# Optimization experiments

Measured on AMD Instinct MI355X. Metric: run time of the kernel, lower is better.

The kernel has to match this reference:

```python
import jax, jax.numpy as jnp
import numpy as np

# Rational/asymptotic approximations for J0, J1 (Abramowitz & Stegun 9.4.x,
# as used in Numerical Recipes), then upward recurrence J2 = (2/x) J1 - J0.
# This reproduces scipy.special.jv(2, x) to ~1e-7 relative accuracy in fp32.

_TWO_OVER_PI = 0.636619772  # 2/pi


def _bessj0(x):
    ax = jnp.abs(x)
    y = x * x
    num = 57568490574.0 + y * (-13362590354.0 + y * (651619640.7
          + y * (-11214424.18 + y * (77392.33017 + y * (-184.9052456)))))
    den = 57568490411.0 + y * (1029532985.0 + y * (9494680.718
          + y * (59272.64853 + y * (267.8532712 + y))))
    small = num / den  # |x| < 8

    ax_safe = jnp.maximum(ax, 1e-20)
    z = 8.0 / ax_safe
    yy = z * z
    xx = ax_safe - 0.785398164  # ax - pi/4
    p1 = 1.0 + yy * (-0.1098628627e-2 + yy * (0.2734510407e-4
         + yy * (-0.2073370639e-5 + yy * 0.2093887211e-6)))
    p2 = -0.1562499995e-1 + yy * (0.1430488765e-3 + yy * (-0.6911147651e-5
         + yy * (0.7621095161e-6 + yy * (-0.934935152e-7))))
    big = jnp.sqrt(_TWO_OVER_PI / ax_safe) * (jnp.cos(xx) * p1 - z * jnp.sin(xx) * p2)
    return jnp.where(ax < 8.0, small, big)


def _bessj1(x):
    ax = jnp.abs(x)
    y = x * x
    num = x * (72362614232.0 + y * (-7895059235.0 + y * (242396853.1
          + y * (-2972611.439 + y * (15704.48260 + y * (-30.16036606))))))
    den = 144725228442.0 + y * (2300535178.0 + y * (18583304.74
          + y * (99447.43394 + y * (376.9991397 + y))))
    small = num / den  # |x| < 8

    ax_safe = jnp.maximum(ax, 1e-20)
    z = 8.0 / ax_safe
    yy = z * z
    xx = ax_safe - 2.356194491  # ax - 3*pi/4
    p1 = 1.0 + yy * (0.183105e-2 + yy * (-0.3516396496e-4
         + yy * (0.2457520174e-5 + yy * (-0.240337019e-6))))
    p2 = 0.04687499995 + yy * (-0.2002690873e-3 + yy * (0.8449199096e-5
         + yy * (-0.88228987e-6 + yy * 0.105787412e-6)))
    big = jnp.sign(x) * jnp.sqrt(_TWO_OVER_PI / ax_safe) * (
        jnp.cos(xx) * p1 - z * jnp.sin(xx) * p2)
    return jnp.where(ax < 8.0, small, big)


def _bessj2(x):
    # J2(x) = (2/x) J1(x) - J0(x); near 0 use leading series J2 ~ x^2/8.
    eps = 1e-4
    ax = jnp.abs(x)
    x_safe = jnp.where(ax < eps, 1.0, x)
    rec = (2.0 / x_safe) * _bessj1(x_safe) - _bessj0(x_safe)
    series = x * x / 8.0
    return jnp.where(ax < eps, series, rec)


def setup_inputs() -> dict:
    key = jax.random.key(0)
    # ~67M elements, 268 MB fp32 -> memory-bound elementwise map
    x = jax.random.uniform(key, (64, 1048576), dtype=jnp.float32,
                           minval=0.0, maxval=30.0)
    return {"x": x}


def reference(x):
    # Original module with type='j2': elementwise jv(2, x)
    return _bessj2(x)
```

## Files before the change

### kernel.cpp

```cpp
#include <hip/hip_runtime.h>


__device__ __forceinline__ float bessj2_fast(float x) {
    float u = 0.25f * x * x;
    float s;
    s = 2.39471e-20f;
    s = fmaf(s, u, -4.02324e-18f);
    s = fmaf(s, u,  5.75284e-16f);
    s = fmaf(s, u, -6.90369e-14f);
    s = fmaf(s, u,  6.83465e-12f);
    s = fmaf(s, u, -5.46772e-10f);
    s = fmaf(s, u,  3.44466e-08f);
    s = fmaf(s, u, -1.65344e-06f);
    s = fmaf(s, u,  5.78704e-05f);
    s = fmaf(s, u, -1.38889e-03f);
    s = fmaf(s, u,  2.08333e-02f);
    s = fmaf(s, u, -1.66667e-01f);
    s = fmaf(s, u,  0.5f);
    float j2_small = u * s;

    float xb   = fmaxf(x, 8.0f);
    float rinv = __builtin_amdgcn_rcpf(xb);
    float z    = 8.0f * rinv;
    float yy   = z * z;
    float amp  = __builtin_amdgcn_sqrtf(0.636619772f * rinv);
    float chi  = xb - 3.92699082f;
    float sc, cc;
    __sincosf(chi, &sc, &cc);
    float p = fmaf(yy, fmaf(yy,  7.74472e-05f, -1.28173828e-02f), 1.0f);
    float q = z * fmaf(yy, fmaf(yy, -1.57318e-05f, 6.00815e-04f), 0.234375f);
    float j2_big = amp * fmaf(cc, p, -(sc * q));

    return (x < 8.0f) ? j2_small : j2_big;
}

__global__ __launch_bounds__(256)
void j2_vec4_kernel(const float* __restrict__ in, float* __restrict__ out,
                    int n4) {
    const float4* in4  = reinterpret_cast<const float4*>(in);
    float4*       out4 = reinterpret_cast<float4*>(out);
    int idx    = blockIdx.x * blockDim.x + threadIdx.x;
    int stride = gridDim.x * blockDim.x;
    for (int i = idx; i < n4; i += stride) {
        float4 v = in4[i];
        float4 r;
        r.x = bessj2_fast(v.x);
        r.y = bessj2_fast(v.y);
        r.z = bessj2_fast(v.z);
        r.w = bessj2_fast(v.w);
        out4[i] = r;
    }
}

__global__ __launch_bounds__(256)
void j2_tail_kernel(const float* __restrict__ in, float* __restrict__ out,
                    int start, int n) {
    int i = start + blockIdx.x * blockDim.x + threadIdx.x;
    if (i < n) out[i] = bessj2_fast(in[i]);
}

extern "C" void kernel_launch(void* const* d_in, const int* in_sizes, int n_in,
                              void* d_out, int out_size, void* d_ws, size_t ws_size,
                              hipStream_t stream) {
    const float* in  = (const float*)d_in[0];
    float*       out = (float*)d_out;
    int n  = in_sizes[0];
    int n4 = n >> 2;

    if (n4 > 0) {
        int blocks = (n4 + 255) / 256;
        if (blocks > 2048) blocks = 2048;
        j2_vec4_kernel<<<blocks, 256, 0, stream>>>(in, out, n4);
    }
    int rem_start = n4 << 2;
    int rem = n - rem_start;
    if (rem > 0) {
        j2_tail_kernel<<<(rem + 255) / 256, 256, 0, stream>>>(in, out,
                                                              rem_start, n);
    }
}
```

Measured before the change: 105.3 us.

## Use nontemporal vector loads/stores, unroll grid-stride loop by two, fold rcp+sqrt into rsq

Switches the streaming loads and stores to nontemporal builtins on native vector types, so the data passes through without polluting caches. The grid-stride loop now processes two float4 chunks per iteration, giving more loads in flight per thread. The amplitude computation replaces a reciprocal plus square root with a single reciprocal square root, and the reciprocal is recovered by squaring it. The rsq-based reciprocal may differ slightly in rounding, and the unroll adds register pressure.

```diff
diff --git a/kernel.cpp b/kernel.cpp
--- a/kernel.cpp
+++ b/kernel.cpp
@@ -1,5 +1,7 @@
 #include <hip/hip_runtime.h>
 
+
+typedef float vf4 __attribute__((ext_vector_type(4)));
 
 __device__ __forceinline__ float bessj2_fast(float x) {
     float u = 0.25f * x * x;
@@ -20,10 +22,11 @@
     float j2_small = u * s;
 
     float xb   = fmaxf(x, 8.0f);
-    float rinv = __builtin_amdgcn_rcpf(xb);
+    float r    = __builtin_amdgcn_rsqf(xb);
+    float rinv = r * r;
+    float amp  = 0.797884561f * r;
     float z    = 8.0f * rinv;
     float yy   = z * z;
-    float amp  = __builtin_amdgcn_sqrtf(0.636619772f * rinv);
     float chi  = xb - 3.92699082f;
     float sc, cc;
     __sincosf(chi, &sc, &cc);
@@ -34,21 +37,35 @@
     return (x < 8.0f) ? j2_small : j2_big;
 }
 
+__device__ __forceinline__ vf4 j2_vec(vf4 v) {
+    vf4 r;
+    r.x = bessj2_fast(v.x);
+    r.y = bessj2_fast(v.y);
+    r.z = bessj2_fast(v.z);
+    r.w = bessj2_fast(v.w);
+    return r;
+}
+
 __global__ __launch_bounds__(256)
 void j2_vec4_kernel(const float* __restrict__ in, float* __restrict__ out,
                     int n4) {
-    const float4* in4  = reinterpret_cast<const float4*>(in);
-    float4*       out4 = reinterpret_cast<float4*>(out);
+    const vf4* in4  = reinterpret_cast<const vf4*>(in);
+    vf4*       out4 = reinterpret_cast<vf4*>(out);
     int idx    = blockIdx.x * blockDim.x + threadIdx.x;
     int stride = gridDim.x * blockDim.x;
-    for (int i = idx; i < n4; i += stride) {
-        float4 v = in4[i];
-        float4 r;
-        r.x = bessj2_fast(v.x);
-        r.y = bessj2_fast(v.y);
-        r.z = bessj2_fast(v.z);
-        r.w = bessj2_fast(v.w);
-        out4[i] = r;
+
+    int i = idx;
+    for (; i + stride < n4; i += 2 * stride) {
+        vf4 a = __builtin_nontemporal_load(in4 + i);
+        vf4 b = __builtin_nontemporal_load(in4 + i + stride);
+        vf4 ra = j2_vec(a);
+        vf4 rb = j2_vec(b);
+        __builtin_nontemporal_store(ra, out4 + i);
+        __builtin_nontemporal_store(rb, out4 + i + stride);
+    }
+    if (i < n4) {
+        vf4 a = __builtin_nontemporal_load(in4 + i);
+        __builtin_nontemporal_store(j2_vec(a), out4 + i);
     }
 }
 
```

New measurement: 100.8 us. 1.04x faster.
